# Kernel tuning notes

Hardware: AMD Instinct MI355X
Metric: run time of the kernel (lower is better)

The kernel has to match this reference:

```python
import jax, jax.numpy as jnp
import numpy as np


def setup_inputs() -> dict:
    key = jax.random.key(0)
    kx, kd = jax.random.split(key)
    B, S, D = 32, 1024, 512
    x = jax.random.normal(kx, (B, S, D), dtype=jnp.float32)
    # per-token repeat counts in [1, 9): mean ~4.5 frames per phoneme
    durations = jax.random.randint(kd, (B, S), 1, 9, dtype=jnp.int32)
    return {"x": x, "durations": durations}


def reference(x, durations):
    """Duration-based token expansion (FastSpeech LengthRegulator).

    Replaces the per-token repeat/cat/pad Python loops with a single
    vectorized gather driven by cumulative duration offsets.
    Returns (expanded_x, mel_len, mel_mask) matching the torch module's
    (expanded_x, target=None, mel_len, mel_mask) with target omitted
    (projection is None in this configuration).
    """
    B, S, D = x.shape
    csum = jnp.cumsum(durations, axis=1)          # [B,S] end offset of each token
    mel_len = csum[:, -1]                         # [B]
    # max_len is data-dependent, same as the torch module's max over batch.
    max_len = int(jax.device_get(jnp.max(mel_len)))
    t = jnp.arange(max_len)                       # [T]
    # output frame t belongs to token j iff csum[j-1] <= t < csum[j]
    idx = jax.vmap(lambda c: jnp.searchsorted(c, t, side="right"))(csum)  # [B,T]
    idx = jnp.minimum(idx, S - 1)                 # clamp padding region
    expanded = jnp.take_along_axis(x, idx[:, :, None], axis=1)  # [B,T,D]
    mel_mask = t[None, :] >= mel_len[:, None]     # [B,T] True where padded
    expanded = jnp.where(mel_mask[:, :, None], jnp.zeros((), x.dtype), expanded)
    return expanded, mel_len, mel_mask
```

## Files before the change

kernel.cpp:

```cpp
#include <hip/hip_runtime.h>
#include <hip/hip_bf16.h>


#define S_TOK 1024
#define B_SZ  32

typedef float vfloat4 __attribute__((ext_vector_type(4)));

__global__ __launch_bounds__(64)
void lr_scan_kernel(const int* __restrict__ dur,
                    int* __restrict__ csum,
                    float* __restrict__ mel_len_out) {
    const int b = blockIdx.x;
    const int lane = threadIdx.x;
    const int* __restrict__ d = dur + b * S_TOK;

    int v[16];
    int sum = 0;
#pragma unroll
    for (int k = 0; k < 16; ++k) {
        v[k] = d[lane * 16 + k];
        sum += v[k];
    }
    int run = 0;
#pragma unroll
    for (int k = 0; k < 16; ++k) { run += v[k]; v[k] = run; }

    int tot = sum;
#pragma unroll
    for (int off = 1; off < 64; off <<= 1) {
        int n = __shfl_up(tot, off, 64);
        if (lane >= off) tot += n;
    }
    const int excl = tot - sum;

#pragma unroll
    for (int k = 0; k < 16; ++k)
        csum[b * S_TOK + lane * 16 + k] = v[k] + excl;
    if (lane == 63) mel_len_out[b] = (float)tot;
}

__global__ __launch_bounds__(128)
void lr_fused_kernel(const float* __restrict__ x,
                     const int* __restrict__ csum,
                     float* __restrict__ out,
                     float* __restrict__ mask,
                     int D, int max_len) {
    const int b = blockIdx.y;
    const int tid = threadIdx.x;
    const int* __restrict__ c = csum + b * S_TOK;
    const int d4 = D >> 2;

    if (blockIdx.x < S_TOK) {
        const int s = blockIdx.x;
        const int base = (s == 0) ? 0 : c[s - 1];
        const int dur = c[s] - base;

        const vfloat4 v =
            ((const vfloat4*)(x + ((size_t)b * S_TOK + s) * (size_t)D))[tid];
        vfloat4* __restrict__ o =
            (vfloat4*)(out + ((size_t)b * max_len + base) * (size_t)D) + tid;
        for (int r = 0; r < dur; ++r)
            __builtin_nontemporal_store(v, o + (size_t)r * d4);
        if (tid < dur)
            mask[(size_t)b * max_len + base + tid] = 0.0f;
    } else {
        const int mel = c[S_TOK - 1];
        const int t0 = mel + (blockIdx.x - S_TOK) * 4;
        if (t0 >= max_len) return;
        const vfloat4 z = (vfloat4)(0.f);
#pragma unroll
        for (int k = 0; k < 4; ++k) {
            const int t = t0 + k;
            if (t < max_len) {
                vfloat4* __restrict__ o =
                    (vfloat4*)(out + ((size_t)b * max_len + t) * (size_t)D) + tid;
                __builtin_nontemporal_store(z, o);
            }
        }
        if (tid < 4 && t0 + tid < max_len)
            mask[(size_t)b * max_len + t0 + tid] = 1.0f;
    }
}

extern "C" void kernel_launch(void* const* d_in, const int* in_sizes, int n_in,
                              void* d_out, int out_size, void* d_ws, size_t ws_size,
                              hipStream_t stream) {
    const float* x = (const float*)d_in[0];
    const int* dur = (const int*)d_in[1];
    float* out = (float*)d_out;

    const int D = in_sizes[0] / in_sizes[1];
    const int max_len = (out_size / B_SZ - 1) / (D + 1);

    int* csum = (int*)d_ws;
    float* mel_len = out + (size_t)B_SZ * max_len * D;
    float* mask = mel_len + B_SZ;

    lr_scan_kernel<<<B_SZ, 64, 0, stream>>>(dur, csum, mel_len);

    const int tail_blocks = (max_len > S_TOK) ? ((max_len - S_TOK + 3) / 4 + 1) : 1;
    dim3 fgrid((unsigned)(S_TOK + tail_blocks), (unsigned)B_SZ);
    lr_fused_kernel<<<fgrid, 128, 0, stream>>>(x, csum, out, mask, D, max_len);
}
```

Measured before the change: 352.5 us.

## Replace per-token scatter with output-tiled gather using LDS binary search

Switches from one block per source token scattering its repeated rows to one block per 64-frame output tile that loads the cumsum into LDS, binary-searches each frame's source token, then gathers rows. Padding and mask writes are folded into the same pass. This is meant to balance work evenly across blocks and remove the variable-length repeat loop and the separate tail blocks. In exchange, x rows are reread once per repeated frame instead of once per token, and each block pays for an LDS load of the cumsum plus the search.

```diff
diff --git a/kernel.cpp b/kernel.cpp
--- a/kernel.cpp
+++ b/kernel.cpp
@@ -1,11 +1,13 @@
 #include <hip/hip_runtime.h>
-#include <hip/hip_bf16.h>
 
 
 #define S_TOK 1024
 #define B_SZ  32
+#define TILE  64
+#define BLK   256
 
 typedef float vfloat4 __attribute__((ext_vector_type(4)));
+typedef int   vint4   __attribute__((ext_vector_type(4)));
 
 __global__ __launch_bounds__(64)
 void lr_scan_kernel(const int* __restrict__ dur,
@@ -40,46 +42,60 @@
     if (lane == 63) mel_len_out[b] = (float)tot;
 }
 
-__global__ __launch_bounds__(128)
-void lr_fused_kernel(const float* __restrict__ x,
-                     const int* __restrict__ csum,
-                     float* __restrict__ out,
-                     float* __restrict__ mask,
-                     int D, int max_len) {
-    const int b = blockIdx.y;
+__global__ __launch_bounds__(BLK)
+void lr_gather_kernel(const float* __restrict__ x,
+                      const int* __restrict__ csum,
+                      float* __restrict__ out,
+                      float* __restrict__ mask,
+                      int D, int max_len) {
+    __shared__ int c_lds[S_TOK];
+    __shared__ int src_lds[TILE];
+
+    const int b   = blockIdx.y;
     const int tid = threadIdx.x;
-    const int* __restrict__ c = csum + b * S_TOK;
-    const int d4 = D >> 2;
+    const int t0  = blockIdx.x * TILE;
 
-    if (blockIdx.x < S_TOK) {
-        const int s = blockIdx.x;
-        const int base = (s == 0) ? 0 : c[s - 1];
-        const int dur = c[s] - base;
+    ((vint4*)c_lds)[tid] = ((const vint4*)(csum + b * S_TOK))[tid];
+    __syncthreads();
+    const int mel = c_lds[S_TOK - 1];
 
-        const vfloat4 v =
-            ((const vfloat4*)(x + ((size_t)b * S_TOK + s) * (size_t)D))[tid];
-        vfloat4* __restrict__ o =
-            (vfloat4*)(out + ((size_t)b * max_len + base) * (size_t)D) + tid;
-        for (int r = 0; r < dur; ++r)
-            __builtin_nontemporal_store(v, o + (size_t)r * d4);
-        if (tid < dur)
-            mask[(size_t)b * max_len + base + tid] = 0.0f;
-    } else {
-        const int mel = c[S_TOK - 1];
-        const int t0 = mel + (blockIdx.x - S_TOK) * 4;
-        if (t0 >= max_len) return;
-        const vfloat4 z = (vfloat4)(0.f);
-#pragma unroll
-        for (int k = 0; k < 4; ++k) {
-            const int t = t0 + k;
-            if (t < max_len) {
-                vfloat4* __restrict__ o =
-                    (vfloat4*)(out + ((size_t)b * max_len + t) * (size_t)D) + tid;
-                __builtin_nontemporal_store(z, o);
+    if (tid < TILE) {
+        const int t = t0 + tid;
+        int src = -1;
+        if (t < mel) {
+            int lo = 0, hi = S_TOK;
+            while (lo < hi) {
+                const int mid = (lo + hi) >> 1;
+                if (c_lds[mid] <= t) lo = mid + 1; else hi = mid;
+            }
+            src = lo;
+        }
+        src_lds[tid] = src;
+        if (t < max_len)
+            mask[(size_t)b * max_len + t] = (t >= mel) ? 1.0f : 0.0f;
+    }
+    __syncthreads();
+
+    const int half = tid >> 7;
+    const int l    = tid & 127;
+    const int d4   = D >> 2;
+    const float* __restrict__ xb = x + (size_t)b * S_TOK * D;
+    float* __restrict__ ob       = out + (size_t)b * max_len * D;
+
+#pragma unroll 4
+    for (int i = 0; i < TILE / 2; ++i) {
+        const int f = 2 * i + half;
+        const int t = t0 + f;
+        if (t < max_len) {
+            const int src = src_lds[f];
+            for (int j = l; j < d4; j += BLK / 2) {
+                vfloat4 v = (vfloat4)(0.f);
+                if (src >= 0)
+                    v = ((const vfloat4*)(xb + (size_t)src * D))[j];
+                __builtin_nontemporal_store(
+                    v, (vfloat4*)(ob + (size_t)t * D) + j);
             }
         }
-        if (tid < 4 && t0 + tid < max_len)
-            mask[(size_t)b * max_len + t0 + tid] = 1.0f;
     }
 }
 
@@ -99,7 +115,6 @@
 
     lr_scan_kernel<<<B_SZ, 64, 0, stream>>>(dur, csum, mel_len);
 
-    const int tail_blocks = (max_len > S_TOK) ? ((max_len - S_TOK + 3) / 4 + 1) : 1;
-    dim3 fgrid((unsigned)(S_TOK + tail_blocks), (unsigned)B_SZ);
-    lr_fused_kernel<<<fgrid, 128, 0, stream>>>(x, csum, out, mask, D, max_len);
+    dim3 ggrid((unsigned)((max_len + TILE - 1) / TILE), (unsigned)B_SZ);
+    lr_gather_kernel<<<ggrid, BLK, 0, stream>>>(x, csum, out, mask, D, max_len);
 }
```

Result: slower. 367.8 us (+4.4%).

## Replace per-token block grid with persistent grid-stride kernel

Applied to the files above, without the earlier changes.

Swaps the 2D grid of one 128-thread block per token for a fixed grid of 2048 blocks of 256 threads. Each block handles two token jobs at a time in a grid-stride loop, and the padding rows are folded into the same loop. The mask is now written in a separate flat grid-stride pass instead of per token. The aim is to cut the cost of launching and scheduling tens of thousands of tiny blocks and to even out the load, at the price of less parallelism while the loop runs and some extra index arithmetic.

```diff
diff --git a/kernel.cpp b/kernel.cpp
--- a/kernel.cpp
+++ b/kernel.cpp
@@ -1,9 +1,10 @@
 #include <hip/hip_runtime.h>
-#include <hip/hip_bf16.h>
 
 
 #define S_TOK 1024
 #define B_SZ  32
+#define BLK   256
+#define GRID2 2048
 
 typedef float vfloat4 __attribute__((ext_vector_type(4)));
 
@@ -40,46 +41,55 @@
     if (lane == 63) mel_len_out[b] = (float)tot;
 }
 
-__global__ __launch_bounds__(128)
-void lr_fused_kernel(const float* __restrict__ x,
-                     const int* __restrict__ csum,
-                     float* __restrict__ out,
-                     float* __restrict__ mask,
-                     int D, int max_len) {
-    const int b = blockIdx.y;
+__global__ __launch_bounds__(BLK)
+void lr_persist_kernel(const float* __restrict__ x,
+                       const int* __restrict__ csum,
+                       float* __restrict__ out,
+                       float* __restrict__ mask,
+                       int D, int max_len, int pad_rows) {
     const int tid = threadIdx.x;
-    const int* __restrict__ c = csum + b * S_TOK;
     const int d4 = D >> 2;
 
-    if (blockIdx.x < S_TOK) {
-        const int s = blockIdx.x;
+    const int total_mask = B_SZ * max_len;
+    for (int idx = blockIdx.x * BLK + tid; idx < total_mask;
+         idx += gridDim.x * BLK) {
+        const int b = idx / max_len;
+        const int t = idx - b * max_len;
+        const int mel = csum[b * S_TOK + S_TOK - 1];
+        mask[idx] = (t >= mel) ? 1.0f : 0.0f;
+    }
+
+    const int half = tid >> 7;
+    const int l    = tid & 127;
+    const int stride = gridDim.x * 2;
+    const int total_tok = B_SZ * S_TOK;
+
+    int job = blockIdx.x * 2 + half;
+    for (; job < total_tok; job += stride) {
+        const int b = job >> 10;
+        const int s = job & (S_TOK - 1);
+        const int* __restrict__ c = csum + b * S_TOK;
         const int base = (s == 0) ? 0 : c[s - 1];
-        const int dur = c[s] - base;
+        const int dur  = c[s] - base;
 
         const vfloat4 v =
-            ((const vfloat4*)(x + ((size_t)b * S_TOK + s) * (size_t)D))[tid];
+            ((const vfloat4*)(x + ((size_t)b * S_TOK + s) * (size_t)D))[l];
         vfloat4* __restrict__ o =
-            (vfloat4*)(out + ((size_t)b * max_len + base) * (size_t)D) + tid;
+            (vfloat4*)(out + ((size_t)b * max_len + base) * (size_t)D) + l;
         for (int r = 0; r < dur; ++r)
             __builtin_nontemporal_store(v, o + (size_t)r * d4);
-        if (tid < dur)
-            mask[(size_t)b * max_len + base + tid] = 0.0f;
-    } else {
-        const int mel = c[S_TOK - 1];
-        const int t0 = mel + (blockIdx.x - S_TOK) * 4;
-        if (t0 >= max_len) return;
-        const vfloat4 z = (vfloat4)(0.f);
-#pragma unroll
-        for (int k = 0; k < 4; ++k) {
-            const int t = t0 + k;
-            if (t < max_len) {
-                vfloat4* __restrict__ o =
-                    (vfloat4*)(out + ((size_t)b * max_len + t) * (size_t)D) + tid;
-                __builtin_nontemporal_store(z, o);
-            }
+    }
+
+    const int total_pad = B_SZ * pad_rows;
+    for (int pj = job - total_tok; pj < total_pad; pj += stride) {
+        const int b = pj / pad_rows;
+        const int k = pj - b * pad_rows;
+        const int t = csum[b * S_TOK + S_TOK - 1] + k;
+        if (t < max_len) {
+            vfloat4* __restrict__ o =
+                (vfloat4*)(out + ((size_t)b * max_len + t) * (size_t)D) + l;
+            __builtin_nontemporal_store((vfloat4)(0.f), o);
         }
-        if (tid < 4 && t0 + tid < max_len)
-            mask[(size_t)b * max_len + t0 + tid] = 1.0f;
     }
 }
 
@@ -99,7 +109,7 @@
 
     lr_scan_kernel<<<B_SZ, 64, 0, stream>>>(dur, csum, mel_len);
 
-    const int tail_blocks = (max_len > S_TOK) ? ((max_len - S_TOK + 3) / 4 + 1) : 1;
-    dim3 fgrid((unsigned)(S_TOK + tail_blocks), (unsigned)B_SZ);
-    lr_fused_kernel<<<fgrid, 128, 0, stream>>>(x, csum, out, mask, D, max_len);
+    const int pad_rows = (max_len > S_TOK) ? (max_len - S_TOK + 1) : 1;
+    lr_persist_kernel<<<GRID2, BLK, 0, stream>>>(x, csum, out, mask,
+                                                 D, max_len, pad_rows);
 }
```

After: 362.9 us. 1.03x slower.
